# Optimization experiments

Hardware: AMD Instinct MI355X
Metric: run time of the kernel (lower is better)

The kernel has to match this reference:

```python
import jax, jax.numpy as jnp
import numpy as np
from math import ceil, sqrt

# Inner module: Linear(2048,4096)+ReLU, Linear(4096,4096)+ReLU, Linear(4096,2048)
D_IN, D_H, D_OUT = 2048, 4096, 2048
BATCH = 4096
# named_modules() order: each Linear yields weight then bias; ReLU skipped
SHAPES = [(D_H, D_IN), (D_H,), (D_H, D_H), (D_H,), (D_OUT, D_H), (D_OUT,)]
NUM_P = sum(int(np.prod(s)) for s in SHAPES)  # 33_566_720
SIZE_N = ceil(sqrt(NUM_P))                    # 5794
SIZE_M = ceil(1.0 * SIZE_N / 2)               # 2897 (compress = 1.0)


def setup_inputs() -> dict:
    key = jax.random.key(0)
    k1, k2, k3 = jax.random.split(key, 3)
    k = sqrt(12) / 2 * SIZE_M ** (-0.25)  # norm_V init bound
    V1 = jax.random.uniform(k1, (SIZE_N, SIZE_M), jnp.float32, -k, k)
    V2 = jax.random.uniform(k2, (SIZE_M, SIZE_N), jnp.float32, -k, k)
    x = jax.random.normal(k3, (BATCH, D_IN), jnp.float32)
    return {"x": x, "V1": V1, "V2": V2}


def _unpack(Vf):
    # scatter-copy: contiguous slices of flattened V -> weights/biases in traversal order
    params, i = [], 0
    for s in SHAPES:
        n = int(np.prod(s))
        params.append(Vf[i:i + n].reshape(s))
        i += n
    return params


def reference(x, V1, V2):
    # WandBtoV: low-rank reconstruction then per-element copy into weights (fused here)
    Vf = (V1 @ V2).reshape(-1)  # [SIZE_N*SIZE_N]; only first NUM_P elements used
    W1, b1, W2, b2, W3, b3 = _unpack(Vf)
    h = jax.nn.relu(x @ W1.T + b1)   # [B, D_H]
    h = jax.nn.relu(h @ W2.T + b2)   # [B, D_H]
    return h @ W3.T + b3             # [B, D_OUT]
```

## Files before the change

### kernel.cpp

```cpp
#include <hip/hip_runtime.h>
#include <stdint.h>

typedef __attribute__((ext_vector_type(8)))  __bf16 bf16x8;
typedef __attribute__((ext_vector_type(16))) float  f32x16;
typedef unsigned short u16;
typedef __attribute__((ext_vector_type(8))) unsigned short u16x8;

#define GLOBAL_AS __attribute__((address_space(1)))
#define LDS_AS    __attribute__((address_space(3)))

__device__ __forceinline__ void load_lds16(const void* g, void* l) {
    __builtin_amdgcn_global_load_lds((const GLOBAL_AS void*)g, (LDS_AS void*)l, 16, 0, 0);
}

__device__ __forceinline__ u16 f2bf(float f) {
    union { float f; uint32_t u; } v; v.f = f;
    uint32_t r = v.u + 0x7FFFu + ((v.u >> 16) & 1u);
    return (u16)(r >> 16);
}
__device__ __forceinline__ float b2f(u16 b) {
    union { uint32_t u; float f; } v; v.u = ((uint32_t)b) << 16;
    return v.f;
}

__global__ void k_conv_pad(const float* __restrict__ in, u16* __restrict__ out,
                           int rIn, int cIn, int cOut, int total8) {
    int idx = blockIdx.x * blockDim.x + threadIdx.x;
    if (idx >= total8) return;
    int c8n = cOut >> 3;
    int r  = idx / c8n;
    int c0 = (idx - r * c8n) << 3;
    u16x8 o;
#pragma unroll
    for (int j = 0; j < 8; ++j) {
        int c = c0 + j;
        o[j] = (r < rIn && c < cIn) ? f2bf(in[(size_t)r * cIn + c]) : (u16)0;
    }
    *(u16x8*)(out + (size_t)r * cOut + c0) = o;
}

__global__ void k_transpose_conv(const float* __restrict__ in, u16* __restrict__ out,
                                 int kIn, int nIn, int kOut) {
    __shared__ float tile[32][33];
    int k0 = blockIdx.x * 32, n0 = blockIdx.y * 32;
    int tx = threadIdx.x, ty = threadIdx.y;
#pragma unroll
    for (int i = 0; i < 4; ++i) {
        int k = k0 + ty + i * 8, n = n0 + tx;
        tile[ty + i * 8][tx] = (k < kIn && n < nIn) ? in[(size_t)k * nIn + n] : 0.f;
    }
    __syncthreads();
#pragma unroll
    for (int i = 0; i < 4; ++i) {
        int n = n0 + ty + i * 8, k = k0 + tx;
        out[(size_t)n * kOut + k] = f2bf(tile[tx][ty + i * 8]);
    }
}

template <int MODE>
__global__ __launch_bounds__(256, 4) void k_gemm_bt(
    const u16* __restrict__ A, const u16* __restrict__ B,
    const u16* __restrict__ bias, void* __restrict__ Cv,
    int K, int ldc, int mReal, int nReal) {
    (void)bias;
    __shared__ __align__(16) char lds[32768];
    char* As = lds;
    char* Bs = lds + 16384;

    const int tid  = threadIdx.x;
    const int w    = tid >> 6, lane = tid & 63;
    const int l31  = lane & 31, hi = lane >> 5;
    const int wm   = (w & 1) * 64, wn = (w >> 1) * 64;
    const int bm   = blockIdx.y * 128, bn = blockIdx.x * 128;

    const int srcRow = tid >> 3;
    const int srcCol = (tid & 7) ^ (srcRow & 7);
    const u16* aSrc = A + (size_t)(bm + srcRow) * K + (srcCol << 3);
    const u16* bSrc = B + (size_t)(bn + srcRow) * K + (srcCol << 3);
    char* aDst = As + ((tid & ~63) << 4);
    char* bDst = Bs + ((tid & ~63) << 4);

    const int aRow0 = (wm + l31) * 128;
    const int aRow1 = (wm + 32 + l31) * 128;
    const int bRow0 = (wn + l31) * 128;
    const int bRow1 = (wn + 32 + l31) * 128;

    f32x16 acc[2][2];
#pragma unroll
    for (int i = 0; i < 2; ++i)
#pragma unroll
        for (int j = 0; j < 2; ++j) acc[i][j] = (f32x16)(0.f);

    for (int k0 = 0; k0 < K; k0 += 64) {
#pragma unroll
        for (int t = 0; t < 4; ++t) {
            load_lds16(aSrc + (size_t)(t * 32) * K, aDst + t * 4096);
            load_lds16(bSrc + (size_t)(t * 32) * K, bDst + t * 4096);
        }
        aSrc += 64; bSrc += 64;
        __syncthreads();
#pragma unroll
        for (int ks = 0; ks < 4; ++ks) {
            const int swz = (((ks * 2 + hi) ^ (l31 & 7)) << 4);
            bf16x8 af[2], bfr[2];
            af[0]  = *(const bf16x8*)(As + aRow0 + swz);
            af[1]  = *(const bf16x8*)(As + aRow1 + swz);
            bfr[0] = *(const bf16x8*)(Bs + bRow0 + swz);
            bfr[1] = *(const bf16x8*)(Bs + bRow1 + swz);
#pragma unroll
            for (int mi = 0; mi < 2; ++mi)
#pragma unroll
                for (int ni = 0; ni < 2; ++ni)
                    acc[mi][ni] = __builtin_amdgcn_mfma_f32_32x32x16_bf16(
                        af[mi], bfr[ni], acc[mi][ni], 0, 0, 0);
        }
        __syncthreads();
    }

    float bv[2];
    if (MODE >= 1) {
#pragma unroll
        for (int ni = 0; ni < 2; ++ni) bv[ni] = b2f(bias[bn + wn + ni * 32 + l31]);
    }
#pragma unroll
    for (int mi = 0; mi < 2; ++mi) {
#pragma unroll
        for (int reg = 0; reg < 16; ++reg) {
            int row = bm + wm + mi * 32 + (reg & 3) + 8 * (reg >> 2) + 4 * hi;
#pragma unroll
            for (int ni = 0; ni < 2; ++ni) {
                int col = bn + wn + ni * 32 + l31;
                float v = acc[mi][ni][reg];
                if (MODE == 0) {
                    if (row < mReal && col < nReal)
                        ((u16*)Cv)[(size_t)row * ldc + col] = f2bf(v);
                } else if (MODE == 1) {
                    v += bv[ni];
                    v = v > 0.f ? v : 0.f;
                    ((u16*)Cv)[(size_t)row * ldc + col] = f2bf(v);
                } else {
                    ((float*)Cv)[(size_t)row * ldc + col] = v + bv[ni];
                }
            }
        }
    }
}


#define BARRIER() do { asm volatile("" ::: "memory"); \
                       __builtin_amdgcn_s_barrier(); \
                       asm volatile("" ::: "memory"); } while (0)
#define LGKM0()   do { asm volatile("s_waitcnt lgkmcnt(0)" ::: "memory"); \
                       __builtin_amdgcn_sched_barrier(0); } while (0)
#define VMCNT0()  do { asm volatile("s_waitcnt vmcnt(0)" ::: "memory"); \
                       __builtin_amdgcn_sched_barrier(0); } while (0)

#define STAGE8(bb, koff) do { \
    _Pragma("unroll") for (int t = 0; t < 4; ++t) \
        load_lds16(aS + (koff) + (size_t)(t * 64) * K, (bb) + wOff + t * 8192); \
    _Pragma("unroll") for (int t = 0; t < 4; ++t) \
        load_lds16(bS + (koff) + (size_t)(t * 64) * K, (bb) + 32768 + wOff + t * 8192); \
} while (0)

#define PH(bb, p, MID) do { \
    const int co_ = chB ^ ((p) << 5); \
    bf16x8 fa0_ = *(const bf16x8*)((bb) + aRowB +     0 + co_); \
    bf16x8 fa1_ = *(const bf16x8*)((bb) + aRowB +  4096 + co_); \
    bf16x8 fa2_ = *(const bf16x8*)((bb) + aRowB +  8192 + co_); \
    bf16x8 fa3_ = *(const bf16x8*)((bb) + aRowB + 12288 + co_); \
    bf16x8 fb0_ = *(const bf16x8*)((bb) + bRowB +     0 + co_); \
    bf16x8 fb1_ = *(const bf16x8*)((bb) + bRowB +  4096 + co_); \
    MID \
    LGKM0(); \
    __builtin_amdgcn_s_setprio(1); \
    acc[0][0] = __builtin_amdgcn_mfma_f32_32x32x16_bf16(fa0_, fb0_, acc[0][0], 0, 0, 0); \
    acc[1][0] = __builtin_amdgcn_mfma_f32_32x32x16_bf16(fa1_, fb0_, acc[1][0], 0, 0, 0); \
    acc[2][0] = __builtin_amdgcn_mfma_f32_32x32x16_bf16(fa2_, fb0_, acc[2][0], 0, 0, 0); \
    acc[3][0] = __builtin_amdgcn_mfma_f32_32x32x16_bf16(fa3_, fb0_, acc[3][0], 0, 0, 0); \
    acc[0][1] = __builtin_amdgcn_mfma_f32_32x32x16_bf16(fa0_, fb1_, acc[0][1], 0, 0, 0); \
    acc[1][1] = __builtin_amdgcn_mfma_f32_32x32x16_bf16(fa1_, fb1_, acc[1][1], 0, 0, 0); \
    acc[2][1] = __builtin_amdgcn_mfma_f32_32x32x16_bf16(fa2_, fb1_, acc[2][1], 0, 0, 0); \
    acc[3][1] = __builtin_amdgcn_mfma_f32_32x32x16_bf16(fa3_, fb1_, acc[3][1], 0, 0, 0); \
    __builtin_amdgcn_s_setprio(0); \
} while (0)

#define PH_PLAIN ;
#define PH_SYNC  LGKM0(); VMCNT0(); BARRIER();

template <int MODE>
__global__ __launch_bounds__(512, 2) void k_gemm256(
    const u16* __restrict__ A, const u16* __restrict__ B,
    const u16* __restrict__ bias, void* __restrict__ Cv,
    int K, int ldc, int mReal, int nReal, int gx, int nTiles) {
    __shared__ __align__(16) char lds[131072];

    const int tid  = threadIdx.x;
    const int w    = tid >> 6, lane = tid & 63;
    const int l31  = lane & 31, hi = lane >> 5;
    const int wr   = w & 1, wc = w >> 1;

    const int cpx = (int)gridDim.x >> 3;
    const int wg0 = ((int)blockIdx.x & 7) * cpx + ((int)blockIdx.x >> 3);

    char* const buf0 = lds;
    char* const buf1 = lds + 65536;

    const int srcRow = tid >> 3;
    const int srcCh  = (tid & 7) ^ (srcRow & 7);
    const int wOff   = (tid & ~63) << 4;

    const int aRowB = (wr * 128 + l31) * 128;
    const int bRowB = 32768 + (wc * 64 + l31) * 128;
    const int chB   = (hi ^ (l31 & 7)) << 4;

    const int nIt = K >> 7;

    for (int v = wg0; v < nTiles; v += (int)gridDim.x) {
        const int bm = (v / gx) * 256;
        const int bn = (v % gx) * 256;
        const u16* const aS = A + (size_t)(bm + srcRow) * K + (srcCh << 3);
        const u16* const bS = B + (size_t)(bn + srcRow) * K + (srcCh << 3);

        f32x16 acc[4][2];
#pragma unroll
        for (int i = 0; i < 4; ++i)
#pragma unroll
            for (int j = 0; j < 2; ++j) acc[i][j] = (f32x16)(0.f);

        STAGE8(buf0, 0);
        VMCNT0();
        BARRIER();

        size_t ko = 0;
#pragma unroll 1
        for (int it = 0; it < nIt; ++it) {
            STAGE8(buf1, ko + 64);
            PH(buf0, 0, PH_PLAIN);
            PH(buf0, 1, PH_PLAIN);
            PH(buf0, 2, PH_PLAIN);
            PH(buf0, 3, PH_SYNC if (it + 1 < nIt) { STAGE8(buf0, ko + 128); });
            PH(buf1, 0, PH_PLAIN);
            PH(buf1, 1, PH_PLAIN);
            PH(buf1, 2, PH_PLAIN);
            PH(buf1, 3, PH_SYNC);
            ko += 128;
        }

        float bv[2];
        if (MODE >= 1) {
#pragma unroll
            for (int ni = 0; ni < 2; ++ni) bv[ni] = b2f(bias[bn + wc * 64 + ni * 32 + l31]);
        }
#pragma unroll
        for (int mi = 0; mi < 4; ++mi) {
#pragma unroll
            for (int reg = 0; reg < 16; ++reg) {
                const int row = bm + wr * 128 + mi * 32 + (reg & 3) + 8 * (reg >> 2) + 4 * hi;
#pragma unroll
                for (int ni = 0; ni < 2; ++ni) {
                    const int col = bn + wc * 64 + ni * 32 + l31;
                    float vv = acc[mi][ni][reg];
                    if (MODE == 0) {
                        if (row < mReal && col < nReal)
                            ((u16*)Cv)[(size_t)row * ldc + col] = f2bf(vv);
                    } else if (MODE == 1) {
                        vv += bv[ni];
                        vv = vv > 0.f ? vv : 0.f;
                        ((u16*)Cv)[(size_t)row * ldc + col] = f2bf(vv);
                    } else {
                        ((float*)Cv)[(size_t)row * ldc + col] = vv + bv[ni];
                    }
                }
            }
        }
    }
}

extern "C" void kernel_launch(void* const* d_in, const int* in_sizes, int n_in,
                              void* d_out, int out_size, void* d_ws, size_t ws_size,
                              hipStream_t stream) {
    (void)in_sizes; (void)n_in; (void)out_size; (void)ws_size;
    const float* x  = (const float*)d_in[0];
    const float* V1 = (const float*)d_in[1];
    const float* V2 = (const float*)d_in[2];

    char* ws = (char*)d_ws;
    u16* Vf   = (u16*)(ws);
    u16* V1b  = (u16*)(ws + 67141120);
    u16* V2bT = (u16*)(ws + 67141120 + 34668544);
    u16* Xb   = (u16*)(ws + 67141120 + 2 * 34668544);
    u16* H1   = V1b;
    u16* H2   = V2bT;

    k_conv_pad<<<8464, 256, 0, stream>>>(V1, V1b, 5794, 2897, 2944, 5888 * 2944 / 8);
    k_transpose_conv<<<dim3(92, 184), dim3(32, 8), 0, stream>>>(V2, V2bT, 2897, 5794, 2944);
    k_conv_pad<<<4096, 256, 0, stream>>>(x, Xb, 4096, 2048, 2048, 4096 * 2048 / 8);

    k_gemm256<0><<<512, 512, 0, stream>>>(V1b, V2bT, nullptr, Vf,
                                          2944, 5794, 5794, 5794, 23, 529);
    k_gemm256<1><<<256, 512, 0, stream>>>(Xb, Vf + 0, Vf + 8388608, H1,
                                          2048, 4096, 4096, 4096, 16, 256);
    k_gemm256<1><<<256, 512, 0, stream>>>(H1, Vf + 8392704, Vf + 25169920, H2,
                                          4096, 4096, 4096, 4096, 16, 256);
    k_gemm_bt<2><<<dim3(16, 32), 256, 0, stream>>>(H2, Vf + 25174016, Vf + 33562624, d_out,
                                                   4096, 2048, 4096, 2048);
}
```

Baseline: 764.7 us.

## Double-buffer LDS fragment reads in registers and use lane-contiguous LDS layout

New measurement: 852.9 us. 11.5% more time.

```diff
diff --git a/kernel.cpp b/kernel.cpp
--- a/kernel.cpp
+++ b/kernel.cpp
@@ -162,30 +162,27 @@
         load_lds16(bS + (koff) + (size_t)(t * 64) * K, (bb) + 32768 + wOff + t * 8192); \
 } while (0)
 
-#define PH(bb, p, MID) do { \
-    const int co_ = chB ^ ((p) << 5); \
-    bf16x8 fa0_ = *(const bf16x8*)((bb) + aRowB +     0 + co_); \
-    bf16x8 fa1_ = *(const bf16x8*)((bb) + aRowB +  4096 + co_); \
-    bf16x8 fa2_ = *(const bf16x8*)((bb) + aRowB +  8192 + co_); \
-    bf16x8 fa3_ = *(const bf16x8*)((bb) + aRowB + 12288 + co_); \
-    bf16x8 fb0_ = *(const bf16x8*)((bb) + bRowB +     0 + co_); \
-    bf16x8 fb1_ = *(const bf16x8*)((bb) + bRowB +  4096 + co_); \
-    MID \
-    LGKM0(); \
+#define RD6(bb, p, FA, FB) do { \
+    FA[0] = *(const bf16x8*)((bb) + aB +     0 + (p) * 1024); \
+    FA[1] = *(const bf16x8*)((bb) + aB +  4096 + (p) * 1024); \
+    FA[2] = *(const bf16x8*)((bb) + aB +  8192 + (p) * 1024); \
+    FA[3] = *(const bf16x8*)((bb) + aB + 12288 + (p) * 1024); \
+    FB[0] = *(const bf16x8*)((bb) + bB +     0 + (p) * 1024); \
+    FB[1] = *(const bf16x8*)((bb) + bB +  4096 + (p) * 1024); \
+} while (0)
+
+#define MM8(FA, FB) do { \
     __builtin_amdgcn_s_setprio(1); \
-    acc[0][0] = __builtin_amdgcn_mfma_f32_32x32x16_bf16(fa0_, fb0_, acc[0][0], 0, 0, 0); \
-    acc[1][0] = __builtin_amdgcn_mfma_f32_32x32x16_bf16(fa1_, fb0_, acc[1][0], 0, 0, 0); \
-    acc[2][0] = __builtin_amdgcn_mfma_f32_32x32x16_bf16(fa2_, fb0_, acc[2][0], 0, 0, 0); \
-    acc[3][0] = __builtin_amdgcn_mfma_f32_32x32x16_bf16(fa3_, fb0_, acc[3][0], 0, 0, 0); \
-    acc[0][1] = __builtin_amdgcn_mfma_f32_32x32x16_bf16(fa0_, fb1_, acc[0][1], 0, 0, 0); \
-    acc[1][1] = __builtin_amdgcn_mfma_f32_32x32x16_bf16(fa1_, fb1_, acc[1][1], 0, 0, 0); \
-    acc[2][1] = __builtin_amdgcn_mfma_f32_32x32x16_bf16(fa2_, fb1_, acc[2][1], 0, 0, 0); \
-    acc[3][1] = __builtin_amdgcn_mfma_f32_32x32x16_bf16(fa3_, fb1_, acc[3][1], 0, 0, 0); \
+    acc[0][0] = __builtin_amdgcn_mfma_f32_32x32x16_bf16(FA[0], FB[0], acc[0][0], 0, 0, 0); \
+    acc[1][0] = __builtin_amdgcn_mfma_f32_32x32x16_bf16(FA[1], FB[0], acc[1][0], 0, 0, 0); \
+    acc[2][0] = __builtin_amdgcn_mfma_f32_32x32x16_bf16(FA[2], FB[0], acc[2][0], 0, 0, 0); \
+    acc[3][0] = __builtin_amdgcn_mfma_f32_32x32x16_bf16(FA[3], FB[0], acc[3][0], 0, 0, 0); \
+    acc[0][1] = __builtin_amdgcn_mfma_f32_32x32x16_bf16(FA[0], FB[1], acc[0][1], 0, 0, 0); \
+    acc[1][1] = __builtin_amdgcn_mfma_f32_32x32x16_bf16(FA[1], FB[1], acc[1][1], 0, 0, 0); \
+    acc[2][1] = __builtin_amdgcn_mfma_f32_32x32x16_bf16(FA[2], FB[1], acc[2][1], 0, 0, 0); \
+    acc[3][1] = __builtin_amdgcn_mfma_f32_32x32x16_bf16(FA[3], FB[1], acc[3][1], 0, 0, 0); \
     __builtin_amdgcn_s_setprio(0); \
 } while (0)
-
-#define PH_PLAIN ;
-#define PH_SYNC  LGKM0(); VMCNT0(); BARRIER();
 
 template <int MODE>
 __global__ __launch_bounds__(512, 2) void k_gemm256(
@@ -205,27 +202,28 @@
     char* const buf0 = lds;
     char* const buf1 = lds + 65536;
 
-    const int srcRow = tid >> 3;
-    const int srcCh  = (tid & 7) ^ (srcRow & 7);
-    const int wOff   = (tid & ~63) << 4;
-
-    const int aRowB = (wr * 128 + l31) * 128;
-    const int bRowB = 32768 + (wc * 64 + l31) * 128;
-    const int chB   = (hi ^ (l31 & 7)) << 4;
+    const int srcRowT = ((w >> 2) * 32) + l31;
+    const int kOffT   = (w & 3) * 16 + (hi << 3);
+    const int wOff    = w * 1024;
+
+    const int aB = wr * 16384 + lane * 16;
+    const int bB = 32768 + wc * 8192 + lane * 16;
 
     const int nIt = K >> 7;
 
     for (int v = wg0; v < nTiles; v += (int)gridDim.x) {
         const int bm = (v / gx) * 256;
         const int bn = (v % gx) * 256;
-        const u16* const aS = A + (size_t)(bm + srcRow) * K + (srcCh << 3);
-        const u16* const bS = B + (size_t)(bn + srcRow) * K + (srcCh << 3);
+        const u16* const aS = A + (size_t)(bm + srcRowT) * K + kOffT;
+        const u16* const bS = B + (size_t)(bn + srcRowT) * K + kOffT;
 
         f32x16 acc[4][2];
 #pragma unroll
         for (int i = 0; i < 4; ++i)
 #pragma unroll
             for (int j = 0; j < 2; ++j) acc[i][j] = (f32x16)(0.f);
+
+        bf16x8 xa[4], xb[2], ya[4], yb[2];
 
         STAGE8(buf0, 0);
         VMCNT0();
@@ -235,14 +233,25 @@
 #pragma unroll 1
         for (int it = 0; it < nIt; ++it) {
             STAGE8(buf1, ko + 64);
-            PH(buf0, 0, PH_PLAIN);
-            PH(buf0, 1, PH_PLAIN);
-            PH(buf0, 2, PH_PLAIN);
-            PH(buf0, 3, PH_SYNC if (it + 1 < nIt) { STAGE8(buf0, ko + 128); });
-            PH(buf1, 0, PH_PLAIN);
-            PH(buf1, 1, PH_PLAIN);
-            PH(buf1, 2, PH_PLAIN);
-            PH(buf1, 3, PH_SYNC);
+            RD6(buf0, 0, xa, xb);
+            RD6(buf0, 1, ya, yb);
+            MM8(xa, xb);
+            RD6(buf0, 2, xa, xb);
+            MM8(ya, yb);
+            RD6(buf0, 3, ya, yb);
+            MM8(xa, xb);
+            LGKM0(); VMCNT0(); BARRIER();
+            if (it + 1 < nIt) { STAGE8(buf0, ko + 128); }
+            MM8(ya, yb);
+            RD6(buf1, 0, xa, xb);
+            RD6(buf1, 1, ya, yb);
+            MM8(xa, xb);
+            RD6(buf1, 2, xa, xb);
+            MM8(ya, yb);
+            RD6(buf1, 3, ya, yb);
+            MM8(xa, xb);
+            LGKM0(); VMCNT0(); BARRIER();
+            MM8(ya, yb);
             ko += 128;
         }
 
```
